# Kernel optimization log

Measured on AMD Instinct MI355X. Metric: run time of the kernel, lower is better.

Reference implementation:

```python
import jax, jax.numpy as jnp
import numpy as np

B = 512; NPG = 50; N = B * NPG          # graphs, nodes per graph, total nodes
EPG = 100; E = B * EPG                   # edges per graph, total edges
SPG = 5; S = B * SPG                     # stems per graph, total stems
DIM = 64; FEAT = 24
CONV_STEPS = 12; S2S_STEPS = 3; NSTEM = 105

lrelu = jax.nn.leaky_relu  # negative_slope 0.01, matches nn.LeakyReLU default

def _lin(k, o, i):
    s = 1.0 / np.sqrt(i)
    return jax.random.uniform(k, (o, i), jnp.float32, -s, s)

def _vec(k, o, i):
    s = 1.0 / np.sqrt(i)
    return jax.random.uniform(k, (o,), jnp.float32, -s, s)

def setup_inputs():
    ks = jax.random.split(jax.random.key(0), 30)
    x = jax.random.normal(ks[0], (N, FEAT), jnp.float32)
    edge_attr = jax.random.uniform(ks[1], (E, 4), jnp.float32)
    gid = jnp.arange(E) // EPG
    src = gid * NPG + jax.random.randint(ks[2], (E,), 0, NPG)
    dst = gid * NPG + jax.random.randint(ks[3], (E,), 0, NPG)
    edge_index = jnp.stack([src, dst]).astype(jnp.int32)
    batch = (jnp.arange(N) // NPG).astype(jnp.int32)
    stems = jax.random.randint(ks[4], (S,), 0, NPG).astype(jnp.int32)
    stems_batch = (jnp.arange(S) // SPG).astype(jnp.int32)
    p = dict(
        lin0_w=_lin(ks[5], DIM, FEAT), lin0_b=_vec(ks[6], DIM, FEAT),
        net1_w=_lin(ks[7], 128, 4), net1_b=_vec(ks[8], 128, 4),
        net2_w=_lin(ks[9], DIM * DIM, 128), net2_b=_vec(ks[10], DIM * DIM, 128),
        root_w=_lin(ks[11], DIM, DIM), conv_b=_vec(ks[12], DIM, DIM),
        gru_wih=_lin(ks[13], 3 * DIM, DIM), gru_whh=_lin(ks[14], 3 * DIM, DIM),
        gru_bih=_vec(ks[15], 3 * DIM, DIM), gru_bhh=_vec(ks[16], 3 * DIM, DIM),
        lin1_w=_lin(ks[17], 8 * DIM, DIM), lin1_b=_vec(ks[18], 8 * DIM, DIM),
        lin2_w=_lin(ks[19], NSTEM, 8 * DIM), lin2_b=_vec(ks[20], NSTEM, 8 * DIM),
        lstm_wih=_lin(ks[21], 4 * DIM, 2 * DIM), lstm_whh=_lin(ks[22], 4 * DIM, DIM),
        lstm_bih=_vec(ks[23], 4 * DIM, 2 * DIM), lstm_bhh=_vec(ks[24], 4 * DIM, DIM),
        lin3_w=_lin(ks[25], 1, 2 * DIM), lin3_b=_vec(ks[26], 1, 2 * DIM),
    )
    return dict(x=x, edge_attr=edge_attr, edge_index=edge_index, batch=batch,
                stems=stems, stems_batch=stems_batch, **p)

def reference(x, edge_attr, edge_index, batch, stems, stems_batch,
              lin0_w, lin0_b, net1_w, net1_b, net2_w, net2_b, root_w, conv_b,
              gru_wih, gru_whh, gru_bih, gru_bhh, lin1_w, lin1_b, lin2_w, lin2_b,
              lstm_wih, lstm_whh, lstm_bih, lstm_bhh, lin3_w, lin3_b):
    src, dst = edge_index[0], edge_index[1]
    out = lrelu(x @ lin0_w.T + lin0_b)        # [N, DIM]
    h = out                                   # GRU hidden state
    # edge-conditioned NNConv weights; edge_attr is constant across the 12 steps,
    # so the edge MLP is evaluated once (same math as re-evaluating per step)
    eh = lrelu(edge_attr @ net1_w.T + net1_b)
    W_e = (eh @ net2_w.T + net2_b).reshape(E, DIM, DIM)  # [E, DIM, DIM]
    deg = jax.ops.segment_sum(jnp.ones(E, x.dtype), dst, num_segments=N)
    inv_deg = (1.0 / jnp.maximum(deg, 1.0))[:, None]
    for _ in range(CONV_STEPS):
        msg = jnp.einsum('ed,edo->eo', out[src], W_e)               # gather + per-edge matvec
        agg = jax.ops.segment_sum(msg, dst, num_segments=N) * inv_deg  # scatter-mean
        m = lrelu(agg + out @ root_w + conv_b)                       # NNConv root + bias
        # single GRU step (torch gate order: r, z, n)
        gi = m @ gru_wih.T + gru_bih
        gh = h @ gru_whh.T + gru_bhh
        r = jax.nn.sigmoid(gi[:, :DIM] + gh[:, :DIM])
        z = jax.nn.sigmoid(gi[:, DIM:2 * DIM] + gh[:, DIM:2 * DIM])
        n = jnp.tanh(gi[:, 2 * DIM:] + r * gh[:, 2 * DIM:])
        h = (1.0 - z) * n + z * h
        out = h
    # per-stem head: data.__slices__['x'][stems_batch] + stems with uniform graphs
    stem_idx = stems_batch * NPG + stems
    stem_x = out[stem_idx]
    per_stem = lrelu(stem_x @ lin1_w.T + lin1_b) @ lin2_w.T + lin2_b  # [S, NSTEM]
    # Set2Set pooling: 3 LSTM-attention steps
    q_star = jnp.zeros((B, 2 * DIM), x.dtype)
    hs = jnp.zeros((B, DIM), x.dtype)
    cs = jnp.zeros((B, DIM), x.dtype)
    for _ in range(S2S_STEPS):
        g = q_star @ lstm_wih.T + lstm_bih + hs @ lstm_whh.T + lstm_bhh
        i_g = jax.nn.sigmoid(g[:, :DIM]); f_g = jax.nn.sigmoid(g[:, DIM:2 * DIM])
        c_g = jnp.tanh(g[:, 2 * DIM:3 * DIM]); o_g = jax.nn.sigmoid(g[:, 3 * DIM:])
        cs = f_g * cs + i_g * c_g
        hs = o_g * jnp.tanh(cs)
        e = jnp.sum(out * hs[batch], axis=-1)                        # [N]
        emax = jax.ops.segment_max(e, batch, num_segments=B)
        a = jnp.exp(e - emax[batch])
        a = a / jax.ops.segment_sum(a, batch, num_segments=B)[batch]  # segment softmax
        r_read = jax.ops.segment_sum(a[:, None] * out, batch, num_segments=B)
        q_star = jnp.concatenate([hs, r_read], axis=1)
    sout = q_star @ lin3_w.T + lin3_b   # [B, 1]
    return (per_stem, sout)
```

## Files before the change

### kernel.cpp

```cpp
#include <hip/hip_runtime.h>
#include <hip/hip_bf16.h>
#include <stdint.h>

#define N_NODES 25600
#define N_EDGES 51200
#define NG      512

typedef __attribute__((ext_vector_type(4))) float f32x4;
typedef __attribute__((ext_vector_type(2))) float f32x2;
typedef __attribute__((ext_vector_type(8))) short bf16x8;

__device__ __forceinline__ float lrelu(float v){ return v > 0.f ? v : 0.01f*v; }
__device__ __forceinline__ float sigm(float v){ return 1.f/(1.f+__expf(-v)); }
__device__ __forceinline__ unsigned short f2b(float v){
  union { float f; uint32_t u; } x; x.f = v;
  uint32_t u = x.u;
  return (unsigned short)((u + 0x7FFFu + ((u>>16)&1u)) >> 16);
}
__device__ __forceinline__ float rl(float v, int l){
  return __int_as_float(__builtin_amdgcn_readlane(__float_as_int(v), l));
}

__global__ void k_prep(const float* __restrict__ net2_w, unsigned short* __restrict__ W2n,
                       const float* __restrict__ gwih, const float* __restrict__ gwhh,
                       float* __restrict__ gw6,
                       const float* __restrict__ lwih, const float* __restrict__ lwhh,
                       float* __restrict__ lwihT, float* __restrict__ lwhhT,
                       const float* __restrict__ lin1w, float* __restrict__ l1T,
                       const float* __restrict__ lin2w, float* __restrict__ l2T,
                       const float* __restrict__ lin0w, float* __restrict__ l0T) {
  const int total = 524288+32768+32768+16384+32768+53760+1536;
  for (int i = blockIdx.x*blockDim.x + threadIdx.x; i < total; i += gridDim.x*blockDim.x) {
    int idx = i;
    if (idx < 524288) {
      int n = idx >> 6, d = idx & 63;
      int k = n >> 6, o = n & 63;
      W2n[idx] = f2b(net2_w[(d*64+o)*128 + k]);
      continue;
    }
    idx -= 524288;
    if (idx < 32768) {
      int dt = idx >> 3, j = idx & 7;
      int d = dt >> 6, t = dt & 63;
      float v = 0.f;
      if (j < 3) v = gwih[(j*64+t)*64 + d];
      else if (j < 6) v = gwhh[((j-3)*64+t)*64 + d];
      gw6[idx] = v; continue;
    }
    idx -= 32768;
    if (idx < 32768) { int c = idx/256, j = idx%256; lwihT[idx] = lwih[j*128+c]; continue; }
    idx -= 32768;
    if (idx < 16384) { int d = idx/256, j = idx%256; lwhhT[idx] = lwhh[j*64+d]; continue; }
    idx -= 16384;
    if (idx < 32768) { int d = idx/512, j = idx%512; l1T[idx] = lin1w[j*64+d]; continue; }
    idx -= 32768;
    if (idx < 53760) { int j = idx/105, o = idx%105; l2T[idx] = lin2w[o*512+j]; continue; }
    idx -= 53760;
    { int f = idx/64, o = idx%64; l0T[idx] = lin0w[o*24+f]; }
  }
}

__global__ __launch_bounds__(256) void k_lin0(const float* __restrict__ x, const float* __restrict__ l0T,
     const float* __restrict__ b, const float* __restrict__ net2_b,
     float* __restrict__ outf, float* __restrict__ Q) {
  int t = threadIdx.x & 63;
  int n = blockIdx.x*4 + (threadIdx.x>>6);
  float xv = (t < 24) ? x[n*24+t] : 0.f;
  float acc = b[t];
  #pragma unroll
  for (int f = 0; f < 24; ++f) acc += __shfl(xv, f) * l0T[f*64+t];
  acc = lrelu(acc);
  outf[n*64+t] = acc;
  float qa = 0.f;
  #pragma unroll 8
  for (int d = 0; d < 64; ++d) qa += __shfl(acc, d) * net2_b[d*64+t];
  Q[n*64+t] = qa;
}

__global__ __launch_bounds__(256) void k_eh(const float* __restrict__ ea, const float* __restrict__ w,
    const float* __restrict__ b, float* __restrict__ ehT) {
  __shared__ float tile[128][65];
  int e0 = blockIdx.x*64;
  int tid = threadIdx.x;
  #pragma unroll
  for (int r = 0; r < 32; ++r) {
    int idx = tid + r*256; int el = idx >> 7, k = idx & 127;
    float4 a = *(const float4*)(ea + (size_t)(e0+el)*4);
    float4 ww = *(const float4*)(w + k*4);
    tile[k][el] = lrelu(a.x*ww.x + a.y*ww.y + a.z*ww.z + a.w*ww.w + b[k]);
  }
  __syncthreads();
  #pragma unroll
  for (int r = 0; r < 32; ++r) {
    int idx = tid + r*256; int k = idx >> 6, el = idx & 63;
    ehT[(size_t)k*N_EDGES + e0 + el] = tile[k][el];
  }
}

__global__ __launch_bounds__(128) void k_csr(const int* __restrict__ ei, int* __restrict__ deg,
                                             int* __restrict__ off, int* __restrict__ csr) {
  __shared__ int cnt[50];
  __shared__ int cur[50];
  __shared__ int dloc[100];
  int g = blockIdx.x, t = threadIdx.x;
  const int* dst = ei + N_EDGES;
  if (t < 50) cnt[t] = 0;
  __syncthreads();
  if (t < 100) { dloc[t] = dst[g*100+t] - g*50; atomicAdd(&cnt[dloc[t]], 1); }
  __syncthreads();
  if (t == 0) { int run = 0; for (int i = 0; i < 50; ++i) { cur[i] = run; run += cnt[i]; } }
  __syncthreads();
  if (t < 50) { deg[g*50+t] = cnt[t]; off[g*50+t] = g*100 + cur[t]; }
  __syncthreads();
  if (t < 100) {
    int p = 0, me = dloc[t];
    for (int i = 0; i < t; ++i) p += (dloc[i] == me);
    csr[g*100 + cur[me] + p] = g*100 + t;
  }
}

__global__ __launch_bounds__(512, 4) void k_step(
    float* __restrict__ outf, const float* __restrict__ ehT,
    const unsigned short* __restrict__ W2n, float* __restrict__ Qb,
    const int* __restrict__ ei, const int* __restrict__ csr,
    const int* __restrict__ offs, const int* __restrict__ deg,
    const float* __restrict__ rootw, const float* __restrict__ conv_b,
    const float* __restrict__ gw6, const float* __restrict__ bih, const float* __restrict__ bhh,
    const float* __restrict__ net2_b) {
  __shared__ __align__(16) char  BtB[128*144];
  __shared__ __align__(16) float Tt[64*132];
  __shared__ __align__(16) char  XbB[64*144];
  __shared__ float ehl[2][256];
  __shared__ int sel[100];
  __shared__ int offl[64];
  __shared__ int degl[64];
  __shared__ float invd[64];
  float* aggL = (float*)BtB;

  const int tid = threadIdx.x;
  const int g = blockIdx.x;
  const int wave = tid >> 6, lane = tid & 63;
  const int t = lane;
  const int q = lane >> 4, cc = lane & 15;
  const int mw = wave >> 1, nh = wave & 1;

  if (tid < 64) {
    int dgv = 0, ofv = 0;
    if (tid < 50) { dgv = deg[g*50+tid]; ofv = offs[g*50+tid] - g*100; }
    degl[tid] = dgv; offl[tid] = ofv;
    invd[tid] = 1.f/(float)(dgv > 0 ? dgv : 1);
  }
  if (tid < 100) {
    int eg = csr[g*100+tid];
    sel[tid] = (ei[eg]-g*50) | ((eg-g*100) << 16);
  }
  for (int i = tid; i < 64*72; i += 512) ((unsigned short*)XbB)[i] = 0;
  __syncthreads();
  for (int i = tid; i < 3200; i += 512) {
    int n = i >> 6, d = i & 63;
    ((unsigned short*)XbB)[n*72+d] = f2b(outf[(size_t)g*3200 + i]);
  }
  __syncthreads();

  bf16x8 xf00, xf01, xf10, xf11;
  {
    int xr0 = nh*32 + cc, xr1 = xr0 + 16;
    xf00 = *(const bf16x8*)(XbB + xr0*144 + (q*8)*2);
    xf01 = *(const bf16x8*)(XbB + xr0*144 + (32+q*8)*2);
    xf10 = *(const bf16x8*)(XbB + xr1*144 + (q*8)*2);
    xf11 = *(const bf16x8*)(XbB + xr1*144 + (32+q*8)*2);
  }

  const int r = tid >> 3, dq = tid & 7;
  const int myo = offl[r], mydg = degl[r];
  const float* ehTg = ehT + (size_t)g*100;
  const int brow = tid >> 2, bpart = tid & 3;

  int4 br0, br1;
  {
    const unsigned short* src = W2n + (size_t)brow*64 + bpart*16;
    br0 = *(const int4*)src; br1 = *(const int4*)(src + 8);
  }
  float er0 = 0.f, er1 = 0.f;
  if (tid < 100) { er0 = ehTg[0*(size_t)N_EDGES + tid]; er1 = ehTg[1*(size_t)N_EDGES + tid]; }
  *(int4*)(BtB + brow*144 + (((bpart*2  )^(brow&7))<<4)) = br0;
  *(int4*)(BtB + brow*144 + (((bpart*2+1)^(brow&7))<<4)) = br1;
  if (tid < 100) { ehl[0][tid*2] = er0; ehl[0][tid*2+1] = er1; }
  __syncthreads();

  float fin0=0.f, fin1=0.f, fin2=0.f, fin3=0.f, fin4=0.f, fin5=0.f, fin6=0.f, fin7=0.f;

  #pragma unroll 1
  for (int c = 0; c < 64; ++c) {
    f32x4 tc00={}, tc01={}, tc10={}, tc11={};
    {
      int ar0 = mw*32 + cc, ar1 = ar0 + 16;
      #pragma unroll
      for (int ks = 0; ks < 2; ++ks) {
        bf16x8 af0 = *(const bf16x8*)(BtB + ar0*144 + (((ks*4+q)^(ar0&7))<<4));
        bf16x8 af1 = *(const bf16x8*)(BtB + ar1*144 + (((ks*4+q)^(ar1&7))<<4));
        bf16x8 xb0 = ks ? xf01 : xf00;
        bf16x8 xb1 = ks ? xf11 : xf10;
        tc00 = __builtin_amdgcn_mfma_f32_16x16x32_bf16(af0, xb0, tc00, 0,0,0);
        tc01 = __builtin_amdgcn_mfma_f32_16x16x32_bf16(af0, xb1, tc01, 0,0,0);
        tc10 = __builtin_amdgcn_mfma_f32_16x16x32_bf16(af1, xb0, tc10, 0,0,0);
        tc11 = __builtin_amdgcn_mfma_f32_16x16x32_bf16(af1, xb1, tc11, 0,0,0);
      }
    }
    {
      int n0a = mw*32 + q*4, n0b = n0a + 16;
      int sA = nh*32 + cc,   sB = sA + 16;
      float4 v;
      v.x=tc00[0]; v.y=tc00[1]; v.z=tc00[2]; v.w=tc00[3];
      *(float4*)&Tt[sA*132 + n0a] = v;
      v.x=tc01[0]; v.y=tc01[1]; v.z=tc01[2]; v.w=tc01[3];
      *(float4*)&Tt[sB*132 + n0a] = v;
      v.x=tc10[0]; v.y=tc10[1]; v.z=tc10[2]; v.w=tc10[3];
      *(float4*)&Tt[sA*132 + n0b] = v;
      v.x=tc11[0]; v.y=tc11[1]; v.z=tc11[2]; v.w=tc11[3];
      *(float4*)&Tt[sB*132 + n0b] = v;
    }
    if (c < 63) {
      const unsigned short* src = W2n + ((size_t)(c+1)*128 + brow)*64 + bpart*16;
      br0 = *(const int4*)src; br1 = *(const int4*)(src + 8);
      if (tid < 100) {
        er0 = ehTg[(size_t)(2*c+2)*N_EDGES + tid];
        er1 = ehTg[(size_t)(2*c+3)*N_EDGES + tid];
      }
    }
    __syncthreads();
    {
      const float* ebuf = ehl[c & 1];
      for (int ii = 0; ii < mydg; ++ii) {
        int pk = sel[myo + ii];
        int s2 = pk & 0xffff, e2 = pk >> 16;
        float ex = ebuf[e2*2], ey = ebuf[e2*2+1];
        const float* tb = &Tt[s2*132];
        float4 ta0 = *(const float4*)(tb + dq*8);
        float4 ta1 = *(const float4*)(tb + dq*8 + 4);
        float4 tb0 = *(const float4*)(tb + 64 + dq*8);
        float4 tb1 = *(const float4*)(tb + 64 + dq*8 + 4);
        fin0 += ex*ta0.x + ey*tb0.x;  fin1 += ex*ta0.y + ey*tb0.y;
        fin2 += ex*ta0.z + ey*tb0.z;  fin3 += ex*ta0.w + ey*tb0.w;
        fin4 += ex*ta1.x + ey*tb1.x;  fin5 += ex*ta1.y + ey*tb1.y;
        fin6 += ex*ta1.z + ey*tb1.z;  fin7 += ex*ta1.w + ey*tb1.w;
      }
    }
    if (c < 63) {
      *(int4*)(BtB + brow*144 + (((bpart*2  )^(brow&7))<<4)) = br0;
      *(int4*)(BtB + brow*144 + (((bpart*2+1)^(brow&7))<<4)) = br1;
      if (tid < 100) { ehl[(c+1)&1][tid*2] = er0; ehl[(c+1)&1][tid*2+1] = er1; }
    }
    __syncthreads();
  }

  {
    for (int ii = 0; ii < mydg; ++ii) {
      int s2 = sel[myo + ii] & 0xffff;
      const float* qp = Qb + (size_t)(g*50 + s2)*64 + dq*8;
      float4 q0 = *(const float4*)(qp);
      float4 q1 = *(const float4*)(qp + 4);
      fin0 += q0.x; fin1 += q0.y; fin2 += q0.z; fin3 += q0.w;
      fin4 += q1.x; fin5 += q1.y; fin6 += q1.z; fin7 += q1.w;
    }
    float4 f0 = {fin0, fin1, fin2, fin3};
    float4 f1 = {fin4, fin5, fin6, fin7};
    *(float4*)&aggL[r*66 + dq*8]     = f0;
    *(float4*)&aggL[r*66 + dq*8 + 4] = f1;
  }
  __syncthreads();

  {
    float ot[8];
    #pragma unroll
    for (int i = 0; i < 8; ++i) {
      int n = wave*8 + i;
      ot[i] = (n < 50) ? outf[(size_t)(g*50+n)*64 + t] : 0.f;
    }
    float mm[8];
    {
      float rc[8] = {0,0,0,0,0,0,0,0};
      for (int d = 0; d < 64; ++d) {
        float w = rootw[d*64+t];
        #pragma unroll
        for (int i = 0; i < 8; ++i) rc[i] += rl(ot[i], d) * w;
      }
      float cb = conv_b[t];
      #pragma unroll
      for (int i = 0; i < 8; ++i) {
        int n = wave*8 + i;
        mm[i] = lrelu(aggL[n*66 + t]*invd[n] + rc[i] + cb);
      }
    }
    float air[8]={}, aiz[8]={}, ain[8]={}, ahr[8]={}, ahz[8]={}, ahn[8]={};
    for (int d = 0; d < 64; ++d) {
      const float* wp = gw6 + (size_t)(d*64+t)*8;
      float4 w0 = *(const float4*)wp;
      float4 w1 = *(const float4*)(wp + 4);
      #pragma unroll
      for (int i = 0; i < 8; ++i) {
        float md = rl(mm[i], d), hd = rl(ot[i], d);
        air[i] += md*w0.x; aiz[i] += md*w0.y; ain[i] += md*w0.z;
        ahr[i] += hd*w0.w; ahz[i] += hd*w1.x; ahn[i] += hd*w1.y;
      }
    }
    float bi0 = bih[t], bi1 = bih[64+t], bi2 = bih[128+t];
    float bh0 = bhh[t], bh1 = bhh[64+t], bh2 = bhh[128+t];
    float h[8];
    #pragma unroll
    for (int i = 0; i < 8; ++i) {
      int n = wave*8 + i;
      float rg = sigm(air[i] + bi0 + ahr[i] + bh0);
      float zg = sigm(aiz[i] + bi1 + ahz[i] + bh1);
      float ng = tanhf(ain[i] + bi2 + rg*(ahn[i] + bh2));
      h[i] = (1.f - zg)*ng + zg*ot[i];
      if (n < 50) outf[(size_t)(g*50+n)*64 + t] = h[i];
    }
    float qa[8] = {0,0,0,0,0,0,0,0};
    for (int d = 0; d < 64; ++d) {
      float qw = net2_b[d*64+t];
      #pragma unroll
      for (int i = 0; i < 8; ++i) qa[i] += rl(h[i], d) * qw;
    }
    #pragma unroll
    for (int i = 0; i < 8; ++i) {
      int n = wave*8 + i;
      if (n < 50) Qb[(size_t)(g*50+n)*64 + t] = qa[i];
    }
  }
}

__global__ __launch_bounds__(256) void k_stem(const float* __restrict__ outf,
    const int* __restrict__ stems, const int* __restrict__ stems_batch,
    const float* __restrict__ l1T, const float* __restrict__ l1b,
    const float* __restrict__ l2T, const float* __restrict__ l2b,
    float* __restrict__ per_stem) {
  int t = threadIdx.x & 63;
  int s = blockIdx.x*4 + (threadIdx.x>>6);
  int node = stems_batch[s]*50 + stems[s];
  float sx = outf[node*64+t];
  float t1[8];
  #pragma unroll
  for (int g = 0; g < 8; ++g) t1[g] = l1b[g*64+t];
  for (int d = 0; d < 64; ++d) {
    float xd = __shfl(sx, d);
    const float* L = l1T + d*512 + t;
    #pragma unroll
    for (int g = 0; g < 8; ++g) t1[g] += xd * L[g*64];
  }
  #pragma unroll
  for (int g = 0; g < 8; ++g) t1[g] = lrelu(t1[g]);
  float a0 = l2b[t];
  float a1 = (t < 41) ? l2b[64+t] : 0.f;
  for (int g = 0; g < 8; ++g) {
    for (int d = 0; d < 64; ++d) {
      float tj = __shfl(t1[g], d);
      int j = g*64 + d;
      a0 += tj * l2T[j*105 + t];
      a1 += tj * ((t < 41) ? l2T[j*105 + 64 + t] : 0.f);
    }
  }
  per_stem[s*105 + t] = a0;
  if (t < 41) per_stem[s*105 + 64 + t] = a1;
}

__global__ __launch_bounds__(64) void k_s2s(const float* __restrict__ outf,
    const float* __restrict__ wihT, const float* __restrict__ whhT,
    const float* __restrict__ bih, const float* __restrict__ bhh,
    const float* __restrict__ l3w, const float* __restrict__ l3b,
    float* __restrict__ sout) {
  int b = blockIdx.x, t = threadIdx.x;
  const float* og = outf + b*50*64;
  float qlo = 0.f, qhi = 0.f, hs = 0.f, cs = 0.f;
  float b0 = bih[t]+bhh[t], b1 = bih[64+t]+bhh[64+t], b2 = bih[128+t]+bhh[128+t], b3 = bih[192+t]+bhh[192+t];
  for (int it = 0; it < 3; ++it) {
    float g0 = b0, g1 = b1, g2 = b2, g3 = b3;
    for (int c = 0; c < 64; ++c) {
      float qc = __shfl(qlo, c);
      const float* L = wihT + c*256 + t;
      g0 += qc*L[0]; g1 += qc*L[64]; g2 += qc*L[128]; g3 += qc*L[192];
    }
    for (int c = 0; c < 64; ++c) {
      float qc = __shfl(qhi, c);
      const float* L = wihT + (64+c)*256 + t;
      g0 += qc*L[0]; g1 += qc*L[64]; g2 += qc*L[128]; g3 += qc*L[192];
    }
    for (int d = 0; d < 64; ++d) {
      float hd = __shfl(hs, d);
      const float* L = whhT + d*256 + t;
      g0 += hd*L[0]; g1 += hd*L[64]; g2 += hd*L[128]; g3 += hd*L[192];
    }
    float ig = sigm(g0), fg = sigm(g1), cg = tanhf(g2), oo = sigm(g3);
    cs = fg*cs + ig*cg;
    hs = oo*tanhf(cs);
    float ei = -3.4e38f;
    for (int i = 0; i < 50; ++i) {
      float p = og[i*64+t]*hs;
      #pragma unroll
      for (int m2 = 1; m2 < 64; m2 <<= 1) p += __shfl_xor(p, m2);
      if (t == i) ei = p;
    }
    float em = ei;
    #pragma unroll
    for (int m2 = 1; m2 < 64; m2 <<= 1) em = fmaxf(em, __shfl_xor(em, m2));
    float av = (t < 50) ? __expf(ei - em) : 0.f;
    float as = av;
    #pragma unroll
    for (int m2 = 1; m2 < 64; m2 <<= 1) as += __shfl_xor(as, m2);
    av /= as;
    float rr = 0.f;
    for (int i = 0; i < 50; ++i) rr += __shfl(av, i) * og[i*64+t];
    qlo = hs; qhi = rr;
  }
  float p = qlo*l3w[t] + qhi*l3w[64+t];
  #pragma unroll
  for (int m2 = 1; m2 < 64; m2 <<= 1) p += __shfl_xor(p, m2);
  if (t == 0) sout[b] = p + l3b[0];
}

extern "C" void kernel_launch(void* const* d_in, const int* in_sizes, int n_in,
                              void* d_out, int out_size, void* d_ws, size_t ws_size,
                              hipStream_t stream) {
  const float* x          = (const float*)d_in[0];
  const float* edge_attr  = (const float*)d_in[1];
  const int*   edge_index = (const int*)  d_in[2];
  const int*   stems      = (const int*)  d_in[4];
  const int*   stems_b    = (const int*)  d_in[5];
  const float* lin0_w = (const float*)d_in[6];
  const float* lin0_b = (const float*)d_in[7];
  const float* net1_w = (const float*)d_in[8];
  const float* net1_b = (const float*)d_in[9];
  const float* net2_w = (const float*)d_in[10];
  const float* net2_b = (const float*)d_in[11];
  const float* root_w = (const float*)d_in[12];
  const float* conv_b = (const float*)d_in[13];
  const float* gru_wih = (const float*)d_in[14];
  const float* gru_whh = (const float*)d_in[15];
  const float* gru_bih = (const float*)d_in[16];
  const float* gru_bhh = (const float*)d_in[17];
  const float* lin1_w = (const float*)d_in[18];
  const float* lin1_b = (const float*)d_in[19];
  const float* lin2_w = (const float*)d_in[20];
  const float* lin2_b = (const float*)d_in[21];
  const float* lstm_wih = (const float*)d_in[22];
  const float* lstm_whh = (const float*)d_in[23];
  const float* lstm_bih = (const float*)d_in[24];
  const float* lstm_bhh = (const float*)d_in[25];
  const float* lin3_w = (const float*)d_in[26];
  const float* lin3_b = (const float*)d_in[27];

  char* ws = (char*)d_ws;
  size_t off = 0;
  auto alloc = [&](size_t bytes) { void* p = ws + off; off += (bytes + 255) & ~(size_t)255; return p; };
  float* ehT  = (float*)alloc((size_t)N_EDGES*128*4);
  unsigned short* W2n = (unsigned short*)alloc(524288*2);
  float* outf = (float*)alloc((size_t)N_NODES*64*4);
  float* Qb   = (float*)alloc((size_t)N_NODES*64*4);
  int* deg  = (int*)alloc(N_NODES*4);
  int* offs = (int*)alloc(N_NODES*4);
  int* csr  = (int*)alloc(N_EDGES*4);
  float* gw6   = (float*)alloc(32768*4);
  float* lwihT = (float*)alloc(32768*4);
  float* lwhhT = (float*)alloc(16384*4);
  float* l1T   = (float*)alloc(32768*4);
  float* l2T   = (float*)alloc(53760*4);
  float* l0T   = (float*)alloc(1536*4);

  if (off > ws_size) {
    hipMemsetAsync(d_out, 0, (size_t)out_size * sizeof(float), stream);
    return;
  }

  float* per_stem = (float*)d_out;
  float* sout = per_stem + 2560*105;

  k_prep<<<2712, 256, 0, stream>>>(net2_w, W2n, gru_wih, gru_whh, gw6,
                                   lstm_wih, lstm_whh, lwihT, lwhhT,
                                   lin1_w, l1T, lin2_w, l2T, lin0_w, l0T);
  k_lin0<<<N_NODES/4, 256, 0, stream>>>(x, l0T, lin0_b, net2_b, outf, Qb);
  k_eh<<<N_EDGES/64, 256, 0, stream>>>(edge_attr, net1_w, net1_b, ehT);
  k_csr<<<NG, 128, 0, stream>>>(edge_index, deg, offs, csr);
  for (int s = 0; s < 12; ++s) {
    k_step<<<NG, 512, 0, stream>>>(outf, ehT, W2n, Qb, edge_index, csr, offs, deg,
                                   root_w, conv_b, gw6, gru_bih, gru_bhh, net2_b);
  }
  k_stem<<<2560/4, 256, 0, stream>>>(outf, stems, stems_b, l1T, lin1_b, l2T, lin2_b, per_stem);
  k_s2s<<<NG, 64, 0, stream>>>(outf, lwihT, lwhhT, lstm_bih, lstm_bhh, lin3_w, lin3_b, sout);
}
```

Before: 2.795 ms.

## Interleave edge-hidden pairs, load node features directly into registers, pack FMA pairs

Edge hidden features are stored as interleaved pairs, so each edge loads its two channels with one 8-byte read per chunk instead of two strided loads. The node feature operand is converted to bf16 straight from global memory into registers with a packed convert instruction, which removes the XbB shared staging buffer and two barriers. The B tile padding is dropped because the XOR swizzle already covers bank conflicts. The first four CSR entries are cached in registers, and the per-edge accumulation uses 2-wide float vectors so packed FMA can be used. Together these reduce shared memory use and instruction count in the hot chunk loop of the 12 repeated step kernels.

```diff
diff --git a/kernel.cpp b/kernel.cpp
--- a/kernel.cpp
+++ b/kernel.cpp
@@ -9,6 +9,8 @@
 typedef __attribute__((ext_vector_type(4))) float f32x4;
 typedef __attribute__((ext_vector_type(2))) float f32x2;
 typedef __attribute__((ext_vector_type(8))) short bf16x8;
+
+typedef union { float4 f4; f32x2 h[2]; } v4u;
 
 __device__ __forceinline__ float lrelu(float v){ return v > 0.f ? v : 0.01f*v; }
 __device__ __forceinline__ float sigm(float v){ return 1.f/(1.f+__expf(-v)); }
@@ -16,6 +18,11 @@
   union { float f; uint32_t u; } x; x.f = v;
   uint32_t u = x.u;
   return (unsigned short)((u + 0x7FFFu + ((u>>16)&1u)) >> 16);
+}
+__device__ __forceinline__ unsigned int pk2(float a, float b){
+  unsigned int r;
+  asm("v_cvt_pk_bf16_f32 %0, %1, %2" : "=v"(r) : "v"(a), "v"(b));
+  return r;
 }
 __device__ __forceinline__ float rl(float v, int l){
   return __int_as_float(__builtin_amdgcn_readlane(__float_as_int(v), l));
@@ -78,7 +85,7 @@
 }
 
 __global__ __launch_bounds__(256) void k_eh(const float* __restrict__ ea, const float* __restrict__ w,
-    const float* __restrict__ b, float* __restrict__ ehT) {
+    const float* __restrict__ b, float* __restrict__ ehP) {
   __shared__ float tile[128][65];
   int e0 = blockIdx.x*64;
   int tid = threadIdx.x;
@@ -93,7 +100,7 @@
   #pragma unroll
   for (int r = 0; r < 32; ++r) {
     int idx = tid + r*256; int k = idx >> 6, el = idx & 63;
-    ehT[(size_t)k*N_EDGES + e0 + el] = tile[k][el];
+    ehP[((size_t)(k>>1)*N_EDGES + e0 + el)*2 + (k&1)] = tile[k][el];
   }
 }
 
@@ -120,22 +127,21 @@
 }
 
 __global__ __launch_bounds__(512, 4) void k_step(
-    float* __restrict__ outf, const float* __restrict__ ehT,
+    float* __restrict__ outf, const float* __restrict__ ehP,
     const unsigned short* __restrict__ W2n, float* __restrict__ Qb,
     const int* __restrict__ ei, const int* __restrict__ csr,
     const int* __restrict__ offs, const int* __restrict__ deg,
     const float* __restrict__ rootw, const float* __restrict__ conv_b,
     const float* __restrict__ gw6, const float* __restrict__ bih, const float* __restrict__ bhh,
     const float* __restrict__ net2_b) {
-  __shared__ __align__(16) char  BtB[128*144];
+  __shared__ __align__(16) char  BtB[128*128];
   __shared__ __align__(16) float Tt[64*132];
-  __shared__ __align__(16) char  XbB[64*144];
-  __shared__ float ehl[2][256];
+  __shared__ f32x2 ehl2[2][112];
   __shared__ int sel[100];
   __shared__ int offl[64];
   __shared__ int degl[64];
   __shared__ float invd[64];
-  float* aggL = (float*)BtB;
+  float* aggL = Tt;
 
   const int tid = threadIdx.x;
   const int g = blockIdx.x;
@@ -154,41 +160,49 @@
     int eg = csr[g*100+tid];
     sel[tid] = (ei[eg]-g*50) | ((eg-g*100) << 16);
   }
-  for (int i = tid; i < 64*72; i += 512) ((unsigned short*)XbB)[i] = 0;
-  __syncthreads();
-  for (int i = tid; i < 3200; i += 512) {
-    int n = i >> 6, d = i & 63;
-    ((unsigned short*)XbB)[n*72+d] = f2b(outf[(size_t)g*3200 + i]);
-  }
-  __syncthreads();
-
-  bf16x8 xf00, xf01, xf10, xf11;
-  {
-    int xr0 = nh*32 + cc, xr1 = xr0 + 16;
-    xf00 = *(const bf16x8*)(XbB + xr0*144 + (q*8)*2);
-    xf01 = *(const bf16x8*)(XbB + xr0*144 + (32+q*8)*2);
-    xf10 = *(const bf16x8*)(XbB + xr1*144 + (q*8)*2);
-    xf11 = *(const bf16x8*)(XbB + xr1*144 + (32+q*8)*2);
-  }
-
-  const int r = tid >> 3, dq = tid & 7;
-  const int myo = offl[r], mydg = degl[r];
-  const float* ehTg = ehT + (size_t)g*100;
   const int brow = tid >> 2, bpart = tid & 3;
-
+  const float* ehPg = ehP + (size_t)g*100*2;
   int4 br0, br1;
   {
     const unsigned short* src = W2n + (size_t)brow*64 + bpart*16;
     br0 = *(const int4*)src; br1 = *(const int4*)(src + 8);
   }
-  float er0 = 0.f, er1 = 0.f;
-  if (tid < 100) { er0 = ehTg[0*(size_t)N_EDGES + tid]; er1 = ehTg[1*(size_t)N_EDGES + tid]; }
-  *(int4*)(BtB + brow*144 + (((bpart*2  )^(brow&7))<<4)) = br0;
-  *(int4*)(BtB + brow*144 + (((bpart*2+1)^(brow&7))<<4)) = br1;
-  if (tid < 100) { ehl[0][tid*2] = er0; ehl[0][tid*2+1] = er1; }
-  __syncthreads();
-
-  float fin0=0.f, fin1=0.f, fin2=0.f, fin3=0.f, fin4=0.f, fin5=0.f, fin6=0.f, fin7=0.f;
+  f32x2 er = {0.f, 0.f};
+  if (tid < 100) er = *(const f32x2*)(ehPg + tid*2);
+  __syncthreads();
+
+  const int r = tid >> 3, dq = tid & 7;
+  const int myo = offl[r], mydg = degl[r];
+  int se0=0, se1=0, se2=0, se3=0;
+  if (mydg > 0) se0 = sel[myo];
+  if (mydg > 1) se1 = sel[myo+1];
+  if (mydg > 2) se2 = sel[myo+2];
+  if (mydg > 3) se3 = sel[myo+3];
+
+  bf16x8 xf00, xf01, xf10, xf11;
+  {
+    int xr0 = nh*32 + cc, xr1 = xr0 + 16;
+    union { bf16x8 v; uint u[4]; } X;
+    #pragma unroll
+    for (int half = 0; half < 4; ++half) {
+      int row = (half & 1) ? xr1 : xr0;
+      int d0  = (half & 2) ? (32 + q*8) : (q*8);
+      if (row < 50) {
+        const float* p = outf + (size_t)(g*50+row)*64 + d0;
+        float4 a = *(const float4*)p;
+        float4 b = *(const float4*)(p+4);
+        X.u[0]=pk2(a.x,a.y); X.u[1]=pk2(a.z,a.w); X.u[2]=pk2(b.x,b.y); X.u[3]=pk2(b.z,b.w);
+      } else { X.u[0]=0; X.u[1]=0; X.u[2]=0; X.u[3]=0; }
+      if (half==0) xf00=X.v; else if (half==1) xf10=X.v; else if (half==2) xf01=X.v; else xf11=X.v;
+    }
+  }
+
+  *(int4*)(BtB + (brow<<7) + (((bpart*2  )^(brow&7))<<4)) = br0;
+  *(int4*)(BtB + (brow<<7) + (((bpart*2+1)^(brow&7))<<4)) = br1;
+  if (tid < 100) ehl2[0][tid] = er;
+  __syncthreads();
+
+  f32x2 fin01={0,0}, fin23={0,0}, fin45={0,0}, fin67={0,0};
 
   #pragma unroll 1
   for (int c = 0; c < 64; ++c) {
@@ -197,8 +211,8 @@
       int ar0 = mw*32 + cc, ar1 = ar0 + 16;
       #pragma unroll
       for (int ks = 0; ks < 2; ++ks) {
-        bf16x8 af0 = *(const bf16x8*)(BtB + ar0*144 + (((ks*4+q)^(ar0&7))<<4));
-        bf16x8 af1 = *(const bf16x8*)(BtB + ar1*144 + (((ks*4+q)^(ar1&7))<<4));
+        bf16x8 af0 = *(const bf16x8*)(BtB + (ar0<<7) + (((ks*4+q)^(ar0&7))<<4));
+        bf16x8 af1 = *(const bf16x8*)(BtB + (ar1<<7) + (((ks*4+q)^(ar1&7))<<4));
         bf16x8 xb0 = ks ? xf01 : xf00;
         bf16x8 xb1 = ks ? xf11 : xf10;
         tc00 = __builtin_amdgcn_mfma_f32_16x16x32_bf16(af0, xb0, tc00, 0,0,0);
@@ -223,48 +237,49 @@
     if (c < 63) {
       const unsigned short* src = W2n + ((size_t)(c+1)*128 + brow)*64 + bpart*16;
       br0 = *(const int4*)src; br1 = *(const int4*)(src + 8);
-      if (tid < 100) {
-        er0 = ehTg[(size_t)(2*c+2)*N_EDGES + tid];
-        er1 = ehTg[(size_t)(2*c+3)*N_EDGES + tid];
-      }
+      if (tid < 100) er = *(const f32x2*)(ehPg + (size_t)(c+1)*N_EDGES*2 + tid*2);
     }
     __syncthreads();
     {
-      const float* ebuf = ehl[c & 1];
+      const f32x2* ebuf = ehl2[c & 1];
       for (int ii = 0; ii < mydg; ++ii) {
-        int pk = sel[myo + ii];
+        int pk = (ii==0)?se0:(ii==1)?se1:(ii==2)?se2:(ii==3)?se3:sel[myo+ii];
         int s2 = pk & 0xffff, e2 = pk >> 16;
-        float ex = ebuf[e2*2], ey = ebuf[e2*2+1];
-        const float* tb = &Tt[s2*132];
-        float4 ta0 = *(const float4*)(tb + dq*8);
-        float4 ta1 = *(const float4*)(tb + dq*8 + 4);
-        float4 tb0 = *(const float4*)(tb + 64 + dq*8);
-        float4 tb1 = *(const float4*)(tb + 64 + dq*8 + 4);
-        fin0 += ex*ta0.x + ey*tb0.x;  fin1 += ex*ta0.y + ey*tb0.y;
-        fin2 += ex*ta0.z + ey*tb0.z;  fin3 += ex*ta0.w + ey*tb0.w;
-        fin4 += ex*ta1.x + ey*tb1.x;  fin5 += ex*ta1.y + ey*tb1.y;
-        fin6 += ex*ta1.z + ey*tb1.z;  fin7 += ex*ta1.w + ey*tb1.w;
+        f32x2 ep = ebuf[e2];
+        const float* tb = &Tt[s2*132 + dq*8];
+        v4u a0, a1, b0, b1;
+        a0.f4 = *(const float4*)(tb);
+        a1.f4 = *(const float4*)(tb + 4);
+        b0.f4 = *(const float4*)(tb + 64);
+        b1.f4 = *(const float4*)(tb + 68);
+        f32x2 ex = {ep.x, ep.x}, ey = {ep.y, ep.y};
+        fin01 += a0.h[0]*ex + b0.h[0]*ey;
+        fin23 += a0.h[1]*ex + b0.h[1]*ey;
+        fin45 += a1.h[0]*ex + b1.h[0]*ey;
+        fin67 += a1.h[1]*ex + b1.h[1]*ey;
       }
     }
     if (c < 63) {
-      *(int4*)(BtB + brow*144 + (((bpart*2  )^(brow&7))<<4)) = br0;
-      *(int4*)(BtB + brow*144 + (((bpart*2+1)^(brow&7))<<4)) = br1;
-      if (tid < 100) { ehl[(c+1)&1][tid*2] = er0; ehl[(c+1)&1][tid*2+1] = er1; }
+      *(int4*)(BtB + (brow<<7) + (((bpart*2  )^(brow&7))<<4)) = br0;
+      *(int4*)(BtB + (brow<<7) + (((bpart*2+1)^(brow&7))<<4)) = br1;
+      if (tid < 100) ehl2[(c+1)&1][tid] = er;
     }
     __syncthreads();
   }
 
   {
     for (int ii = 0; ii < mydg; ++ii) {
-      int s2 = sel[myo + ii] & 0xffff;
+      int pk = (ii==0)?se0:(ii==1)?se1:(ii==2)?se2:(ii==3)?se3:sel[myo+ii];
+      int s2 = pk & 0xffff;
       const float* qp = Qb + (size_t)(g*50 + s2)*64 + dq*8;
-      float4 q0 = *(const float4*)(qp);
-      float4 q1 = *(const float4*)(qp + 4);
-      fin0 += q0.x; fin1 += q0.y; fin2 += q0.z; fin3 += q0.w;
-      fin4 += q1.x; fin5 += q1.y; fin6 += q1.z; fin7 += q1.w;
-    }
-    float4 f0 = {fin0, fin1, fin2, fin3};
-    float4 f1 = {fin4, fin5, fin6, fin7};
+      v4u q0, q1;
+      q0.f4 = *(const float4*)(qp);
+      q1.f4 = *(const float4*)(qp + 4);
+      fin01 += q0.h[0]; fin23 += q0.h[1];
+      fin45 += q1.h[0]; fin67 += q1.h[1];
+    }
+    float4 f0 = {fin01.x, fin01.y, fin23.x, fin23.y};
+    float4 f1 = {fin45.x, fin45.y, fin67.x, fin67.y};
     *(float4*)&aggL[r*66 + dq*8]     = f0;
     *(float4*)&aggL[r*66 + dq*8 + 4] = f1;
   }
@@ -452,7 +467,7 @@
   char* ws = (char*)d_ws;
   size_t off = 0;
   auto alloc = [&](size_t bytes) { void* p = ws + off; off += (bytes + 255) & ~(size_t)255; return p; };
-  float* ehT  = (float*)alloc((size_t)N_EDGES*128*4);
+  float* ehP  = (float*)alloc((size_t)N_EDGES*128*4);
   unsigned short* W2n = (unsigned short*)alloc(524288*2);
   float* outf = (float*)alloc((size_t)N_NODES*64*4);
   float* Qb   = (float*)alloc((size_t)N_NODES*64*4);
@@ -478,10 +493,10 @@
                                    lstm_wih, lstm_whh, lwihT, lwhhT,
                                    lin1_w, l1T, lin2_w, l2T, lin0_w, l0T);
   k_lin0<<<N_NODES/4, 256, 0, stream>>>(x, l0T, lin0_b, net2_b, outf, Qb);
-  k_eh<<<N_EDGES/64, 256, 0, stream>>>(edge_attr, net1_w, net1_b, ehT);
+  k_eh<<<N_EDGES/64, 256, 0, stream>>>(edge_attr, net1_w, net1_b, ehP);
   k_csr<<<NG, 128, 0, stream>>>(edge_index, deg, offs, csr);
   for (int s = 0; s < 12; ++s) {
-    k_step<<<NG, 512, 0, stream>>>(outf, ehT, W2n, Qb, edge_index, csr, offs, deg,
+    k_step<<<NG, 512, 0, stream>>>(outf, ehP, W2n, Qb, edge_index, csr, offs, deg,
                                    root_w, conv_b, gw6, gru_bih, gru_bhh, net2_b);
   }
   k_stem<<<2560/4, 256, 0, stream>>>(outf, stems, stems_b, l1T, lin1_b, l2T, lin2_b, per_stem);
```

Result: faster. 2.516 ms (-10.0%).
